# Optimization experiments

Measured on AMD Instinct MI355X. Metric: run time of the kernel, lower is better.

Reference implementation:

```python
import jax, jax.numpy as jnp
import numpy as np


def _rotated_kernels(kernel, n_or):
    """Nearest-neighbour rotated copies of the kernel.

    kernel: [C, kOr, kH, kW] -> returns [n_or, C, kOr, kH, kW] where slice t is the
    kernel sampled at R_{2*pi*t/n_or}(y', x') about the kernel center; rotated
    coordinates that fall outside the kernel grid contribute zero.
    """
    C, kOr, kH, kW = kernel.shape
    cy = (kH - 1) / 2.0
    cx = (kW - 1) / 2.0
    ang = 2.0 * jnp.pi * jnp.arange(n_or, dtype=jnp.float32) / n_or
    ca = jnp.cos(ang)[:, None, None]  # [n_or,1,1]
    sa = jnp.sin(ang)[:, None, None]
    yy = jnp.arange(kH, dtype=jnp.float32)[:, None] - cy  # [kH,1]
    xx = jnp.arange(kW, dtype=jnp.float32)[None, :] - cx  # [1,kW]
    # rotate grid points by angle theta
    ys = sa * xx + ca * yy  # [n_or,kH,kW]
    xs = ca * xx - sa * yy
    iy = jnp.round(ys + cy).astype(jnp.int32)
    ix = jnp.round(xs + cx).astype(jnp.int32)
    mask = ((iy >= 0) & (iy < kH) & (ix >= 0) & (ix < kW)).astype(kernel.dtype)
    iyc = jnp.clip(iy, 0, kH - 1)
    ixc = jnp.clip(ix, 0, kW - 1)
    rot = kernel[:, :, iyc, ixc]            # [C,kOr,n_or,kH,kW] (gather)
    rot = rot * mask[None, None]            # zero out-of-grid samples
    return jnp.transpose(rot, (2, 0, 1, 3, 4))  # [n_or,C,kOr,kH,kW]


def setup_inputs() -> dict:
    key = jax.random.key(0)
    k1, k2 = jax.random.split(key)
    B, C, Or, H, W = 8, 32, 8, 128, 128
    kOr, kH, kW = 8, 5, 5
    x = jax.random.normal(k1, (B, C, Or, H, W), dtype=jnp.float32)
    # module parameter: uniform(-1, 1) per reset_parameters()
    kernel = jax.random.uniform(k2, (C, kOr, kH, kW), minval=-1.0, maxval=1.0,
                                dtype=jnp.float32)
    return {"x": x, "kernel": kernel}


def reference(x, kernel):
    """SE(2) linear (depthwise) group convolution.

    out[b,c,t,y,x] = sum_{t',y',x'} x[b,c,(t+t')%Or, y+y', x+x']
                     * kernel[c, t', NN(R_{2pi t/Or}(y', x'))]
    with centered, zero-padded spatial offsets ('SAME').
    """
    B, C, Or, H, W = x.shape
    _, kOr, kH, kW = kernel.shape
    rotk = _rotated_kernels(kernel, Or)  # [Or,C,kOr,kH,kW]
    dn = ('NCHW', 'OIHW', 'NCHW')
    out = jnp.zeros((B, C * Or, H, W), dtype=x.dtype)
    for tp in range(kOr):  # small fixed orientation-offset loop
        xs = jnp.roll(x, -tp, axis=2).reshape(B, C * Or, H, W)  # circular wrap in Or
        k = jnp.transpose(rotk[:, :, tp], (1, 0, 2, 3)).reshape(C * Or, 1, kH, kW)
        out = out + jax.lax.conv_general_dilated(
            xs, k, window_strides=(1, 1), padding='SAME',
            feature_group_count=C * Or, dimension_numbers=dn)
    return out.reshape(B, C, Or, H, W)
```

## Files before the change

### kernel.cpp

```cpp
#include <hip/hip_runtime.h>


typedef short bf16x8 __attribute__((ext_vector_type(8)));
typedef float f32x4 __attribute__((ext_vector_type(4)));

__device__ inline unsigned short f2bf(float f) {
    unsigned int u = __float_as_uint(f);
    u += 0x7fffu + ((u >> 16) & 1u);
    return (unsigned short)(u >> 16);
}
__device__ inline unsigned pk2(float a, float b) {
    return (unsigned)f2bf(a) | ((unsigned)f2bf(b) << 16);
}

__device__ __constant__ float CA8[8] = {1.0f, 0.70710678f, 0.0f, -0.70710678f,
                                        -1.0f, -0.70710678f, 0.0f, 0.70710678f};
__device__ __constant__ float SA8[8] = {0.0f, 0.70710678f, 1.0f, 0.70710678f,
                                        0.0f, -0.70710678f, -1.0f, -0.70710678f};

__global__ __launch_bounds__(256)
void se2_mfma(const float* __restrict__ x, const float* __restrict__ kern,
              float* __restrict__ out) {
    __shared__ __align__(16) unsigned short ldsx[36 * 36 * 8];
    __shared__ __align__(16) unsigned short ldsw[8 * 28 * 8];

    const int bid = (blockIdx.x & 7) * 512 + (blockIdx.x >> 3);
    const int tx = bid & 3, ty = (bid >> 2) & 3;
    const int bc = bid >> 4;
    const int c  = bc & 31;
    const int X0 = tx * 32, Y0 = ty * 32;
    const int tid = threadIdx.x;

    for (int e = tid; e < 1792; e += 256) {
        int t   = e / 224;
        int rem = e - t * 224;
        int tap = rem >> 3;
        int o   = rem & 7;
        float w = 0.0f;
        if (tap < 25) {
            int dy = tap / 5, dx = tap - 5 * (tap / 5);
            float ca = CA8[t], sa = SA8[t];
            float xx = (float)dx - 2.0f, yy = (float)dy - 2.0f;
            int iy = (int)rintf(sa * xx + ca * yy + 2.0f);
            int ix = (int)rintf(ca * xx - sa * yy + 2.0f);
            if (iy >= 0 && iy < 5 && ix >= 0 && ix < 5) {
                int tp = (o - t) & 7;
                w = kern[(c * 8 + tp) * 25 + iy * 5 + ix];
            }
        }
        ldsw[e] = f2bf(w);
    }

    const float* xbase = x + (size_t)bc * 131072;
    for (int e = tid; e < 1296; e += 256) {
        int r  = e / 36, cc2 = e - r * 36;
        int gy = Y0 - 2 + r, gx = X0 - 2 + cc2;
        float v[8];
        if (gy >= 0 && gy < 128 && gx >= 0 && gx < 128) {
            const float* src = xbase + gy * 128 + gx;
#pragma unroll
            for (int o = 0; o < 8; ++o) v[o] = src[o * 16384];
        } else {
#pragma unroll
            for (int o = 0; o < 8; ++o) v[o] = 0.0f;
        }
        *reinterpret_cast<uint4*>(&ldsx[e * 8]) =
            make_uint4(pk2(v[0], v[1]), pk2(v[2], v[3]),
                       pk2(v[4], v[5]), pk2(v[6], v[7]));
    }
    __syncthreads();

    const int lane  = tid & 63;
    const int wv    = tid >> 6;
    const int g     = lane >> 4;
    const int col16 = lane & 15;

    bf16x8 wfrag[7];
    int    tapoff[7];
    const bf16x8 zfrag = {0, 0, 0, 0, 0, 0, 0, 0};
#pragma unroll
    for (int cc = 0; cc < 7; ++cc) {
        int tap  = cc * 4 + g;
        int tapc = tap < 25 ? tap : 24;
        int dy = tapc / 5, dx = tapc - 5 * (tapc / 5);
        tapoff[cc] = (dy * 36 + dx) * 8;
        wfrag[cc] = (col16 < 8)
            ? *reinterpret_cast<const bf16x8*>(&ldsw[(col16 * 28 + tap) * 8])
            : zfrag;
    }

    float* outl = out + (size_t)bc * 131072 + (size_t)col16 * 16384 +
                  (size_t)Y0 * 128 + X0 + g * 4;

#pragma unroll 1
    for (int ct = 0; ct < 16; ++ct) {
        int y  = wv * 8 + (ct >> 1);
        int xh = ct & 1;
        int baseS = (y * 36 + xh * 16 + col16) * 8;
        f32x4 acc = {0.f, 0.f, 0.f, 0.f};
#pragma unroll
        for (int cc = 0; cc < 7; ++cc) {
            bf16x8 xf = *reinterpret_cast<const bf16x8*>(&ldsx[baseS + tapoff[cc]]);
            acc = __builtin_amdgcn_mfma_f32_16x16x32_bf16(xf, wfrag[cc], acc, 0, 0, 0);
        }
        if (col16 < 8)
            *reinterpret_cast<float4*>(outl + (size_t)y * 128 + xh * 16) =
                make_float4(acc[0], acc[1], acc[2], acc[3]);
    }
}

extern "C" void kernel_launch(void* const* d_in, const int* in_sizes, int n_in,
                              void* d_out, int out_size, void* d_ws, size_t ws_size,
                              hipStream_t stream) {
    const float* x    = (const float*)d_in[0];
    const float* kern = (const float*)d_in[1];
    float* out = (float*)d_out;
    dim3 grid(4096), block(256);
    se2_mfma<<<grid, block, 0, stream>>>(x, kern, out);
}
```

Before: 58.36 us.

## Double-buffer input tiles in LDS and loop over x-tiles per block

Each block now handles a 16-row strip across four 32-wide x-tiles instead of one 32x32 tile, and the grid is halved. The next x-tile's input is loaded into registers while MFMA work on the current tile runs, then packed into a second LDS buffer, so global-load latency overlaps with compute. This trades a larger halo fraction (16+4 rows) and higher register pressure for fewer blocks and overlapped loads.

```diff
diff --git a/kernel.cpp b/kernel.cpp
--- a/kernel.cpp
+++ b/kernel.cpp
@@ -3,6 +3,8 @@
 
 typedef short bf16x8 __attribute__((ext_vector_type(8)));
 typedef float f32x4 __attribute__((ext_vector_type(4)));
+
+#define NCH 720
 
 __device__ inline unsigned short f2bf(float f) {
     unsigned int u = __float_as_uint(f);
@@ -21,14 +23,14 @@
 __global__ __launch_bounds__(256)
 void se2_mfma(const float* __restrict__ x, const float* __restrict__ kern,
               float* __restrict__ out) {
-    __shared__ __align__(16) unsigned short ldsx[36 * 36 * 8];
+    __shared__ __align__(16) unsigned short ldsx[2][NCH * 8];
     __shared__ __align__(16) unsigned short ldsw[8 * 28 * 8];
 
-    const int bid = (blockIdx.x & 7) * 512 + (blockIdx.x >> 3);
-    const int tx = bid & 3, ty = (bid >> 2) & 3;
-    const int bc = bid >> 4;
+    const int bid = (blockIdx.x & 7) * 256 + (blockIdx.x >> 3);
+    const int ys = bid & 7;
+    const int bc = bid >> 3;
     const int c  = bc & 31;
-    const int X0 = tx * 32, Y0 = ty * 32;
+    const int Y0 = ys * 16;
     const int tid = threadIdx.x;
 
     for (int e = tid; e < 1792; e += 256) {
@@ -50,12 +52,13 @@
         }
         ldsw[e] = f2bf(w);
     }
+    __syncthreads();
 
     const float* xbase = x + (size_t)bc * 131072;
-    for (int e = tid; e < 1296; e += 256) {
-        int r  = e / 36, cc2 = e - r * 36;
-        int gy = Y0 - 2 + r, gx = X0 - 2 + cc2;
-        float v[8];
+
+    auto loadch = [&](int xt, int e, float (&v)[8]) {
+        int r = e / 36, col = e - r * 36;
+        int gy = Y0 - 2 + r, gx = xt * 32 - 2 + col;
         if (gy >= 0 && gy < 128 && gx >= 0 && gx < 128) {
             const float* src = xbase + gy * 128 + gx;
 #pragma unroll
@@ -64,11 +67,12 @@
 #pragma unroll
             for (int o = 0; o < 8; ++o) v[o] = 0.0f;
         }
-        *reinterpret_cast<uint4*>(&ldsx[e * 8]) =
+    };
+    auto packch = [&](int buf, int e, const float (&v)[8]) {
+        *reinterpret_cast<uint4*>(&ldsx[buf][e * 8]) =
             make_uint4(pk2(v[0], v[1]), pk2(v[2], v[3]),
                        pk2(v[4], v[5]), pk2(v[6], v[7]));
-    }
-    __syncthreads();
+    };
 
     const int lane  = tid & 63;
     const int wv    = tid >> 6;
@@ -89,23 +93,55 @@
             : zfrag;
     }
 
-    float* outl = out + (size_t)bc * 131072 + (size_t)col16 * 16384 +
-                  (size_t)Y0 * 128 + X0 + g * 4;
+    float* outl = out + (size_t)bc * 131072 + (size_t)col16 * 16384 + g * 4;
 
+    auto compute = [&](int buf, int xt, int half) {
+#pragma unroll
+        for (int j = 0; j < 4; ++j) {
+            int ct = half * 4 + j;
+            int yl = wv * 4 + (ct >> 1);
+            int xh = ct & 1;
+            int baseS = (yl * 36 + xh * 16 + col16) * 8;
+            const unsigned short* px = &ldsx[buf][0];
+            f32x4 acc = {0.f, 0.f, 0.f, 0.f};
+#pragma unroll
+            for (int cc = 0; cc < 7; ++cc) {
+                bf16x8 xf = *reinterpret_cast<const bf16x8*>(&px[baseS + tapoff[cc]]);
+                acc = __builtin_amdgcn_mfma_f32_16x16x32_bf16(xf, wfrag[cc], acc, 0, 0, 0);
+            }
+            if (col16 < 8)
+                *reinterpret_cast<float4*>(outl + (size_t)(Y0 + yl) * 128 +
+                                           xt * 32 + xh * 16) =
+                    make_float4(acc[0], acc[1], acc[2], acc[3]);
+        }
+    };
+
+    float s0[8], s1[8], s2[8];
+    const bool has2 = (tid < NCH - 512);
+
+    loadch(0, tid, s0);
+    loadch(0, tid + 256, s1);
+    if (has2) loadch(0, tid + 512, s2);
+    packch(0, tid, s0);
+    packch(0, tid + 256, s1);
+    if (has2) packch(0, tid + 512, s2);
+    __syncthreads();
+
+    int cur = 0;
 #pragma unroll 1
-    for (int ct = 0; ct < 16; ++ct) {
-        int y  = wv * 8 + (ct >> 1);
-        int xh = ct & 1;
-        int baseS = (y * 36 + xh * 16 + col16) * 8;
-        f32x4 acc = {0.f, 0.f, 0.f, 0.f};
-#pragma unroll
-        for (int cc = 0; cc < 7; ++cc) {
-            bf16x8 xf = *reinterpret_cast<const bf16x8*>(&ldsx[baseS + tapoff[cc]]);
-            acc = __builtin_amdgcn_mfma_f32_16x16x32_bf16(xf, wfrag[cc], acc, 0, 0, 0);
+    for (int xt = 0; xt < 4; ++xt) {
+        const bool pre = (xt < 3);
+        if (pre) { loadch(xt + 1, tid, s0); loadch(xt + 1, tid + 256, s1); }
+        compute(cur, xt, 0);
+        if (pre) {
+            packch(cur ^ 1, tid, s0);
+            packch(cur ^ 1, tid + 256, s1);
+            if (has2) loadch(xt + 1, tid + 512, s2);
         }
-        if (col16 < 8)
-            *reinterpret_cast<float4*>(outl + (size_t)y * 128 + xh * 16) =
-                make_float4(acc[0], acc[1], acc[2], acc[3]);
+        compute(cur, xt, 1);
+        if (pre && has2) packch(cur ^ 1, tid + 512, s2);
+        __syncthreads();
+        cur ^= 1;
     }
 }
 
@@ -115,6 +151,6 @@
     const float* x    = (const float*)d_in[0];
     const float* kern = (const float*)d_in[1];
     float* out = (float*)d_out;
-    dim3 grid(4096), block(256);
+    dim3 grid(2048), block(256);
     se2_mfma<<<grid, block, 0, stream>>>(x, kern, out);
 }
```

Result: slower. 63.41 us (+8.7%).

## Software-pipeline halo loads, overlap with weight setup, and dual-accumulator MFMA loop

Applied to the files above, without the earlier changes.

Adds a barrier after the weight table is built, then unrolls the input halo staging into explicit two-register load/pack stages so that global loads for later chunks are in flight while earlier chunks are packed to LDS, and so that the first loads overlap the weight-fragment reads. The compute loop now handles both 16-wide halves of a row per iteration with two independent accumulators, giving the MFMA unit two interleaved dependency chains. It also sets a minimum-blocks hint of 5 in launch bounds to limit register use. The cost is more live registers, which the occupancy hint may cap and cause spilling, plus an extra barrier.

```diff
diff --git a/kernel.cpp b/kernel.cpp
--- a/kernel.cpp
+++ b/kernel.cpp
@@ -18,7 +18,7 @@
 __device__ __constant__ float SA8[8] = {0.0f, 0.70710678f, 1.0f, 0.70710678f,
                                         0.0f, -0.70710678f, -1.0f, -0.70710678f};
 
-__global__ __launch_bounds__(256)
+__global__ __launch_bounds__(256, 5)
 void se2_mfma(const float* __restrict__ x, const float* __restrict__ kern,
               float* __restrict__ out) {
     __shared__ __align__(16) unsigned short ldsx[36 * 36 * 8];
@@ -50,12 +50,13 @@
         }
         ldsw[e] = f2bf(w);
     }
+    __syncthreads();
 
     const float* xbase = x + (size_t)bc * 131072;
-    for (int e = tid; e < 1296; e += 256) {
-        int r  = e / 36, cc2 = e - r * 36;
-        int gy = Y0 - 2 + r, gx = X0 - 2 + cc2;
-        float v[8];
+
+    auto loadch = [&](int e, float (&v)[8]) {
+        int r = e / 36, col = e - r * 36;
+        int gy = Y0 - 2 + r, gx = X0 - 2 + col;
         if (gy >= 0 && gy < 128 && gx >= 0 && gx < 128) {
             const float* src = xbase + gy * 128 + gx;
 #pragma unroll
@@ -64,16 +65,22 @@
 #pragma unroll
             for (int o = 0; o < 8; ++o) v[o] = 0.0f;
         }
+    };
+    auto packch = [&](int e, const float (&v)[8]) {
         *reinterpret_cast<uint4*>(&ldsx[e * 8]) =
             make_uint4(pk2(v[0], v[1]), pk2(v[2], v[3]),
                        pk2(v[4], v[5]), pk2(v[6], v[7]));
-    }
-    __syncthreads();
+    };
 
     const int lane  = tid & 63;
     const int wv    = tid >> 6;
     const int g     = lane >> 4;
     const int col16 = lane & 15;
+
+    float sA[8], sB[8];
+
+    loadch(tid, sA);
+    loadch(tid + 256, sB);
 
     bf16x8 wfrag[7];
     int    tapoff[7];
@@ -89,23 +96,39 @@
             : zfrag;
     }
 
+    packch(tid, sA);
+    packch(tid + 256, sB);
+    loadch(tid + 512, sA);
+    loadch(tid + 768, sB);
+    packch(tid + 512, sA);
+    packch(tid + 768, sB);
+    loadch(tid + 1024, sA);
+    if (tid < 16) loadch(tid + 1280, sB);
+    packch(tid + 1024, sA);
+    if (tid < 16) packch(tid + 1280, sB);
+    __syncthreads();
+
     float* outl = out + (size_t)bc * 131072 + (size_t)col16 * 16384 +
                   (size_t)Y0 * 128 + X0 + g * 4;
 
-#pragma unroll 1
-    for (int ct = 0; ct < 16; ++ct) {
-        int y  = wv * 8 + (ct >> 1);
-        int xh = ct & 1;
-        int baseS = (y * 36 + xh * 16 + col16) * 8;
-        f32x4 acc = {0.f, 0.f, 0.f, 0.f};
+#pragma unroll 2
+    for (int cp = 0; cp < 8; ++cp) {
+        int y = wv * 8 + cp;
+        int baseS = (y * 36 + col16) * 8;
+        f32x4 acc0 = {0.f, 0.f, 0.f, 0.f};
+        f32x4 acc1 = {0.f, 0.f, 0.f, 0.f};
 #pragma unroll
         for (int cc = 0; cc < 7; ++cc) {
-            bf16x8 xf = *reinterpret_cast<const bf16x8*>(&ldsx[baseS + tapoff[cc]]);
-            acc = __builtin_amdgcn_mfma_f32_16x16x32_bf16(xf, wfrag[cc], acc, 0, 0, 0);
+            bf16x8 xf0 = *reinterpret_cast<const bf16x8*>(&ldsx[baseS + tapoff[cc]]);
+            bf16x8 xf1 = *reinterpret_cast<const bf16x8*>(&ldsx[baseS + 128 + tapoff[cc]]);
+            acc0 = __builtin_amdgcn_mfma_f32_16x16x32_bf16(xf0, wfrag[cc], acc0, 0, 0, 0);
+            acc1 = __builtin_amdgcn_mfma_f32_16x16x32_bf16(xf1, wfrag[cc], acc1, 0, 0, 0);
         }
-        if (col16 < 8)
-            *reinterpret_cast<float4*>(outl + (size_t)y * 128 + xh * 16) =
-                make_float4(acc[0], acc[1], acc[2], acc[3]);
+        if (col16 < 8) {
+            float* po = outl + (size_t)y * 128;
+            *reinterpret_cast<float4*>(po)      = make_float4(acc0[0], acc0[1], acc0[2], acc0[3]);
+            *reinterpret_cast<float4*>(po + 16) = make_float4(acc1[0], acc1[1], acc1[2], acc1[3]);
+        }
     }
 }
 
```

After: 56.73 us. 1.03x faster.
